# Kernel optimization log

Measured on AMD Instinct MI355X. Metric: run time of the kernel, lower is better.

The kernel has to match this reference:

```python
import jax, jax.numpy as jnp
import numpy as np

EPS = 1e-12


def _cosine_cost_volume(ref, tgt, D):
    """PSMNet-style shifted cosine-correlation cost volume, num_groups=1.
    ref, tgt: [B, C, Hf, Wf] quarter-res features. Returns [B, 1, D, Hf, Wf];
    positions w < d are 0 (zero-padded target -> zero cosine)."""
    B, C, Hf, Wf = ref.shape
    rn = ref * jax.lax.rsqrt(jnp.sum(ref * ref, axis=1, keepdims=True) + EPS)
    tn = tgt * jax.lax.rsqrt(jnp.sum(tgt * tgt, axis=1, keepdims=True) + EPS)
    pad = jnp.pad(tn, ((0, 0), (0, 0), (0, 0), (D - 1, 0)))  # left zero-pad

    def one_disp(d):
        t = jax.lax.dynamic_slice_in_dim(pad, D - 1 - d, Wf, axis=3)
        return jnp.sum(rn * t, axis=1)  # [B, Hf, Wf]

    vol = jax.vmap(one_disp)(jnp.arange(D))  # [D, B, Hf, Wf]
    return jnp.transpose(vol, (1, 0, 2, 3))[:, None]  # [B, 1, D, Hf, Wf]


def setup_inputs() -> dict:
    key = jax.random.key(0)
    k1, k2 = jax.random.split(key)
    B, C, Hf, Wf = 1, 32, 96, 192  # quarter-res ViT features (out_feats=32)
    left_fea = jax.random.normal(k1, (B, C, Hf, Wf), dtype=jnp.float32)
    right_fea = jax.random.normal(k2, (B, C, Hf, Wf), dtype=jnp.float32)
    return {"left_fea": left_fea, "right_fea": right_fea, "H": 384, "W": 768, "maxdisp": 192}


def reference(left_fea, right_fea, H, W, maxdisp):
    B = left_fea.shape[0]
    # training-branch cost volume (W//4 disparity levels, not detached in source)
    cost_init = _cosine_cost_volume(left_fea, right_fea, W // 4)
    # inference path: maxdisp//4 levels, trilinear upsample to [maxdisp, H, W]
    cost = _cosine_cost_volume(left_fea, right_fea, maxdisp // 4)
    cost = jax.lax.stop_gradient(cost)
    cost_up = jax.image.resize(cost, (B, 1, maxdisp, H, W), method="trilinear")
    pred = jnp.argmax(cost_up, axis=2)  # [B, 1, H, W]
    pred = jnp.maximum(pred, 1).astype(jnp.float32)  # pred[pred<1]=1
    return cost_init, pred
```

## Files before the change

### kernel.cpp

```cpp
#include <hip/hip_runtime.h>
#include <math.h>

#define HF 96
#define WF 192
#define CC 32
#define NPIX (HF*WF)
#define DFULL 192
#define DQ 48
#define HO 384
#define WO 768
#define SR 200

__global__ __launch_bounds__(256) void kcost(const float* __restrict__ L,
                                             const float* __restrict__ R,
                                             float* __restrict__ out) {
    __shared__ __align__(16) float Ls[CC * WF];
    __shared__ __align__(16) float Rb[CC * SR];
    const int h = blockIdx.x;
    const int tid = threadIdx.x;

    for (int i = tid; i < CC * 4; i += 256) Rb[(i >> 2) * SR + (i & 3)] = 0.0f;

    if (tid < WF) {
        const int w = tid;
        float lr[CC], rr[CC];
        float sl = 0.0f, sr = 0.0f;
        #pragma unroll
        for (int c = 0; c < CC; ++c) {
            float lv = L[c * NPIX + h * WF + w];
            float rv = R[c * NPIX + h * WF + w];
            lr[c] = lv; rr[c] = rv;
            sl = fmaf(lv, lv, sl);
            sr = fmaf(rv, rv, sr);
        }
        const float il = 1.0f / sqrtf(sl + 1e-12f);
        const float ir = 1.0f / sqrtf(sr + 1e-12f);
        #pragma unroll
        for (int c = 0; c < CC; ++c) {
            Ls[c * WF + w] = lr[c] * il;
            Rb[c * SR + 4 + w] = rr[c] * ir;
        }
    }
    __syncthreads();

    const int t = blockIdx.y * 256 + tid;
    if (t >= 1176) return;

    const int u = 1175 - t;
    int wu = (int)((sqrtf(8.0f * (float)u + 1.0f) - 1.0f) * 0.5f);
    while ((wu + 1) * (wu + 2) / 2 <= u) ++wu;
    while (wu * (wu + 1) / 2 > u) --wu;
    const int du = u - wu * (wu + 1) / 2;
    const int wt = 47 - du;
    const int dt = 47 - wu;

    const int w0 = wt * 4, d0 = dt * 4;
    const int base = w0 - d0;

    float a00=0,a01=0,a02=0,a03=0;
    float a10=0,a11=0,a12=0,a13=0;
    float a20=0,a21=0,a22=0,a23=0;
    float a30=0,a31=0,a32=0,a33=0;

    #pragma unroll 4
    for (int c = 0; c < CC; ++c) {
        const float4 lv = *(const float4*)&Ls[c * WF + w0];
        const float4 r0 = *(const float4*)&Rb[c * SR + base];
        const float4 r1 = *(const float4*)&Rb[c * SR + base + 4];
        a00 = fmaf(lv.x, r1.x, a00); a01 = fmaf(lv.y, r1.y, a01);
        a02 = fmaf(lv.z, r1.z, a02); a03 = fmaf(lv.w, r1.w, a03);
        a10 = fmaf(lv.x, r0.w, a10); a11 = fmaf(lv.y, r1.x, a11);
        a12 = fmaf(lv.z, r1.y, a12); a13 = fmaf(lv.w, r1.z, a13);
        a20 = fmaf(lv.x, r0.z, a20); a21 = fmaf(lv.y, r0.w, a21);
        a22 = fmaf(lv.z, r1.x, a22); a23 = fmaf(lv.w, r1.y, a23);
        a30 = fmaf(lv.x, r0.y, a30); a31 = fmaf(lv.y, r0.z, a31);
        a32 = fmaf(lv.z, r0.w, a32); a33 = fmaf(lv.w, r1.x, a33);
    }

    {
        float4 v;
        v.x=a00; v.y=a01; v.z=a02; v.w=a03;
        *(float4*)&out[(d0 + 0) * NPIX + h * WF + w0] = v;
        v.x=a10; v.y=a11; v.z=a12; v.w=a13;
        *(float4*)&out[(d0 + 1) * NPIX + h * WF + w0] = v;
        v.x=a20; v.y=a21; v.z=a22; v.w=a23;
        *(float4*)&out[(d0 + 2) * NPIX + h * WF + w0] = v;
        v.x=a30; v.y=a31; v.z=a32; v.w=a33;
        *(float4*)&out[(d0 + 3) * NPIX + h * WF + w0] = v;
    }

    if (wt > dt) {
        const int za = (wt - dt - 1) * 4;
        const int zb = (47 - dt) * 4;
        const float4 z = {0.0f, 0.0f, 0.0f, 0.0f};
        #pragma unroll
        for (int j = 0; j < 4; ++j)
            *(float4*)&out[(zb + j) * NPIX + h * WF + za] = z;
    }
}

__global__ __launch_bounds__(256) void kpred(const float* __restrict__ cost,
                                             float* __restrict__ pred) {
    const int mIdx = blockIdx.x * 64 + threadIdx.x;
    const int h = blockIdx.y * 4 + threadIdx.y;
    if (mIdx > 192) return;
    const int m = mIdx - 1;

    float sh = (float)(2 * h - 3) * 0.125f;
    float fh = sh - floorf(sh);
    int h0 = (int)floorf(sh);
    int h1 = h0 + 1;
    if (h0 < 0)      { h0 = 0; h1 = 0; fh = 0.0f; }
    if (h1 > HF - 1) { h1 = HF - 1;    fh = 0.0f; }
    const float wh0 = 1.0f - fh, wh1 = fh;

    const bool edge = (m < 0) || (m >= WF - 1);
    const int w0 = (m < 0) ? 0 : ((m >= WF - 1) ? WF - 1 : m);
    const int w1 = (m < 0) ? 0 : ((m >= WF - 1) ? WF - 1 : m + 1);

    float fr[4];
    #pragma unroll
    for (int r = 0; r < 4; ++r) fr[r] = edge ? 0.0f : (0.125f + 0.25f * (float)r);

    const int i00 = h0 * WF + w0;
    const int i10 = h1 * WF + w0;
    const int i01 = h0 * WF + w1;
    const int i11 = h1 * WF + w1;

    float bp[4], best[4];
    int bi[4];
    {
        const float* s = cost;
        float q00 = s[i00], q10 = s[i10], q01 = s[i01], q11 = s[i11];
        float A0 = fmaf(wh1, q10, wh0 * q00);
        float A1 = fmaf(wh1, q11, wh0 * q01);
        #pragma unroll
        for (int r = 0; r < 4; ++r) {
            bp[r] = fmaf(fr[r], A1, (1.0f - fr[r]) * A0);
            best[r] = bp[r];
            bi[r] = 0;
        }
    }

    for (int k = 1; k < DQ; ++k) {
        const float* s = cost + k * NPIX;
        float q00 = s[i00], q10 = s[i10], q01 = s[i01], q11 = s[i11];
        float A0 = fmaf(wh1, q10, wh0 * q00);
        float A1 = fmaf(wh1, q11, wh0 * q01);
        #pragma unroll
        for (int r = 0; r < 4; ++r) {
            float b = fmaf(fr[r], A1, (1.0f - fr[r]) * A0);
            float cand; int ci;
            if (b > bp[r]) { cand = fmaf(0.875f, b, 0.125f * bp[r]); ci = 4 * k + 1; }
            else           { cand = fmaf(0.125f, b, 0.875f * bp[r]); ci = 4 * k - 2; }
            if (cand > best[r]) { best[r] = cand; bi[r] = ci; }
            bp[r] = b;
        }
    }
    #pragma unroll
    for (int r = 0; r < 4; ++r)
        if (bp[r] > best[r]) bi[r] = 190;

    float v[4];
    #pragma unroll
    for (int r = 0; r < 4; ++r) v[r] = (float)(bi[r] < 1 ? 1 : bi[r]);

    float* prow = pred + h * WO;
    if (m < 0) {
        float2 o; o.x = v[0]; o.y = v[0];
        *(float2*)&prow[0] = o;
    } else if (m >= WF - 1) {
        float2 o; o.x = v[0]; o.y = v[0];
        *(float2*)&prow[WO - 2] = o;
    } else {
        float2 o0; o0.x = v[0]; o0.y = v[1];
        float2 o1; o1.x = v[2]; o1.y = v[3];
        *(float2*)&prow[4 * m + 2] = o0;
        *(float2*)&prow[4 * m + 4] = o1;
    }
}

extern "C" void kernel_launch(void* const* d_in, const int* in_sizes, int n_in,
                              void* d_out, int out_size, void* d_ws, size_t ws_size,
                              hipStream_t stream) {
    const float* L = (const float*)d_in[0];
    const float* R = (const float*)d_in[1];
    float* out = (float*)d_out;
    float* pred = out + DFULL * NPIX;

    kcost<<<dim3(HF, 5), 256, 0, stream>>>(L, R, out);
    kpred<<<dim3(4, HF), dim3(64, 4), 0, stream>>>(out, pred);
}
```

Before: 99.66 us.

## Split argmax disparity chain across 8 lanes with shuffle reduction in kpred

The per-pixel serial loop over 48 disparity levels in the prediction kernel is split across 8 lanes, each handling about 6 levels with one overlapping level, and the lanes combine partial argmax results with xor shuffles that break ties toward the lower index. This raises parallelism and memory-level parallelism, since kpred previously launched only about 18k threads running long dependent load chains. In exchange, every lane reloads the overlap level, adds shuffle work, and the launch grid is reshaped to one flat dimension.

```diff
diff --git a/kernel.cpp b/kernel.cpp
--- a/kernel.cpp
+++ b/kernel.cpp
@@ -101,9 +101,11 @@
 
 __global__ __launch_bounds__(256) void kpred(const float* __restrict__ cost,
                                              float* __restrict__ pred) {
-    const int mIdx = blockIdx.x * 64 + threadIdx.x;
-    const int h = blockIdx.y * 4 + threadIdx.y;
-    if (mIdx > 192) return;
+    const int tid = threadIdx.x;
+    const int lane = tid & 7;
+    const int chainId = blockIdx.x * 32 + (tid >> 3);
+    const int h = chainId / 193;
+    const int mIdx = chainId - h * 193;
     const int m = mIdx - 1;
 
     float sh = (float)(2 * h - 3) * 0.125f;
@@ -127,39 +129,62 @@
     const int i01 = h0 * WF + w1;
     const int i11 = h1 * WF + w1;
 
+    const int base = 6 * lane;
+    float A0v[7], A1v[7];
+    #pragma unroll
+    for (int t = 0; t < 7; ++t) {
+        int s = base + t;
+        if (s > 47) s = 47;
+        const float* sp = cost + s * NPIX;
+        const float q00 = sp[i00], q10 = sp[i10], q01 = sp[i01], q11 = sp[i11];
+        A0v[t] = fmaf(wh1, q10, wh0 * q00);
+        A1v[t] = fmaf(wh1, q11, wh0 * q01);
+    }
+
     float bp[4], best[4];
     int bi[4];
-    {
-        const float* s = cost;
-        float q00 = s[i00], q10 = s[i10], q01 = s[i01], q11 = s[i11];
-        float A0 = fmaf(wh1, q10, wh0 * q00);
-        float A1 = fmaf(wh1, q11, wh0 * q01);
+    #pragma unroll
+    for (int r = 0; r < 4; ++r) {
+        const float b0 = fmaf(fr[r], A1v[0], (1.0f - fr[r]) * A0v[0]);
+        bp[r] = b0;
+        if (lane == 0) { best[r] = b0;        bi[r] = 0; }
+        else           { best[r] = -INFINITY; bi[r] = 0x7fffffff; }
+    }
+
+    #pragma unroll
+    for (int t = 1; t < 7; ++t) {
+        const int k = base + t;
+        const bool valid = (k <= 47);
         #pragma unroll
         for (int r = 0; r < 4; ++r) {
-            bp[r] = fmaf(fr[r], A1, (1.0f - fr[r]) * A0);
-            best[r] = bp[r];
-            bi[r] = 0;
-        }
-    }
-
-    for (int k = 1; k < DQ; ++k) {
-        const float* s = cost + k * NPIX;
-        float q00 = s[i00], q10 = s[i10], q01 = s[i01], q11 = s[i11];
-        float A0 = fmaf(wh1, q10, wh0 * q00);
-        float A1 = fmaf(wh1, q11, wh0 * q01);
-        #pragma unroll
-        for (int r = 0; r < 4; ++r) {
-            float b = fmaf(fr[r], A1, (1.0f - fr[r]) * A0);
+            const float b = fmaf(fr[r], A1v[t], (1.0f - fr[r]) * A0v[t]);
             float cand; int ci;
             if (b > bp[r]) { cand = fmaf(0.875f, b, 0.125f * bp[r]); ci = 4 * k + 1; }
             else           { cand = fmaf(0.125f, b, 0.875f * bp[r]); ci = 4 * k - 2; }
-            if (cand > best[r]) { best[r] = cand; bi[r] = ci; }
+            if (valid && cand > best[r]) { best[r] = cand; bi[r] = ci; }
             bp[r] = b;
         }
     }
-    #pragma unroll
-    for (int r = 0; r < 4; ++r)
-        if (bp[r] > best[r]) bi[r] = 190;
+
+    if (lane == 7) {
+        #pragma unroll
+        for (int r = 0; r < 4; ++r)
+            if (bp[r] > best[r]) { best[r] = bp[r]; bi[r] = 190; }
+    }
+
+    #pragma unroll
+    for (int mask = 1; mask < 8; mask <<= 1) {
+        #pragma unroll
+        for (int r = 0; r < 4; ++r) {
+            const float ov = __shfl_xor(best[r], mask, 8);
+            const int   oi = __shfl_xor(bi[r],   mask, 8);
+            if (ov > best[r] || (ov == best[r] && oi < bi[r])) {
+                best[r] = ov; bi[r] = oi;
+            }
+        }
+    }
+
+    if (lane != 0) return;
 
     float v[4];
     #pragma unroll
@@ -189,5 +214,5 @@
     float* pred = out + DFULL * NPIX;
 
     kcost<<<dim3(HF, 5), 256, 0, stream>>>(L, R, out);
-    kpred<<<dim3(4, HF), dim3(64, 4), 0, stream>>>(out, pred);
+    kpred<<<dim3(2316), 256, 0, stream>>>(out, pred);
 }
```

Result: faster. 97.56 us (-2.1%).
